# Performance work log

Measured on AMD Instinct MI355X. Metric: run time of the kernel, lower is better.

Reference implementation:

```python
import jax, jax.numpy as jnp
import numpy as np

B, S, H = 32, 512, 768
NH, HD = 8, 96
NC = 3
SEP = 102
NEG = -1e9


def telu(x):
    return x * jnp.tanh(jnp.exp(x))


def setup_inputs() -> dict:
    rng = np.random.default_rng(0)
    key = jax.random.key(0)
    ks = jax.random.split(key, 16)
    # ragged premise/hypothesis spans: [CLS] premise [SEP] hypothesis [SEP] pad
    s1 = rng.integers(64, 256, size=B)
    s2 = rng.integers(s1 + 32, 500)
    ids = rng.integers(1000, 30000, size=(B, S))  # avoid accidental SEP ids
    for i in range(B):
        ids[i, 0] = 101
        ids[i, s1[i]] = SEP
        ids[i, s2[i]] = SEP
        ids[i, s2[i] + 1:] = 0
    pos = np.arange(S)[None, :]
    am = (pos <= s2[:, None]).astype(np.int32)

    def lin(k, i, o):
        return jax.random.normal(k, (i, o), jnp.float32) * 0.02

    return dict(
        hidden_states=jax.random.normal(ks[0], (B, S, H), jnp.float32),
        input_ids=jnp.asarray(ids, jnp.int32),
        attention_mask=jnp.asarray(am, jnp.int32),
        fe_w1=lin(ks[1], H, 512), fe_b1=jnp.zeros(512), fe_g=jnp.ones(512), fe_be=jnp.zeros(512),
        fe_w2=lin(ks[2], 512, 128), fe_b2=jnp.zeros(128),
        al_w1=lin(ks[3], 2 * H, 768), al_b1=jnp.zeros(768),
        al_w2=lin(ks[4], 768, 128), al_b2=jnp.zeros(128),
        mha_wq=lin(ks[5], H, H), mha_bq=jnp.zeros(H),
        mha_wk=lin(ks[6], H, H), mha_bk=jnp.zeros(H),
        mha_wv=lin(ks[7], H, H), mha_bv=jnp.zeros(H),
        mha_wo=lin(ks[8], H, H), mha_bo=jnp.zeros(H),
        dp_w=lin(ks[9], H, 128), dp_b=jnp.zeros(128),
        ap_w=lin(ks[10], H, 128), ap_b=jnp.zeros(128),
        cl_w1=lin(ks[11], 512, 64), cl_b1=jnp.zeros(64),
        cl_w2=lin(ks[12], 64, NC), cl_b2=jnp.zeros(NC),
    )


def reference(hidden_states, input_ids, attention_mask,
              fe_w1, fe_b1, fe_g, fe_be, fe_w2, fe_b2,
              al_w1, al_b1, al_w2, al_b2,
              mha_wq, mha_bq, mha_wk, mha_bk, mha_wv, mha_bv, mha_wo, mha_bo,
              dp_w, dp_b, ap_w, ap_b, cl_w1, cl_b1, cl_w2, cl_b2):
    hs = hidden_states
    am = attention_mask.astype(hs.dtype)
    sep = (input_ids == SEP)
    pos = jnp.arange(S)[None, :]
    s1 = jnp.argmax(sep, axis=1)            # first SEP
    s2 = (S - 1) - jnp.argmax(sep[:, ::-1], axis=1)  # second SEP
    prem = ((pos >= 1) & (pos < s1[:, None])).astype(hs.dtype)   # premise span [1, s1)
    hyp = ((pos > s1[:, None]) & (pos < s2[:, None])).astype(hs.dtype)  # hypothesis (s1, s2)

    def mmean(x, m):  # masked mean over seq: x [B,S,H], m [B,S]
        return jnp.einsum('bsh,bs->bh', x, m) / jnp.clip(m.sum(1, keepdims=True), 1e-9, None)

    # pooled + mean + max representations -> feature_extractor
    pooled = hs[:, 0]
    mean_rep = mmean(hs, am)
    max_rep = jnp.max(jnp.where(am[..., None] > 0, hs, NEG), axis=1)
    h = (pooled + mean_rep + max_rep) @ fe_w1 + fe_b1
    h = (h - h.mean(-1, keepdims=True)) / jnp.sqrt(h.var(-1, keepdims=True) + 1e-5) * fe_g + fe_be
    feat = telu(h @ fe_w2 + fe_b2)

    # sentence diff head
    sent_diff = jnp.abs(mmean(hs, prem) - mmean(hs, hyp))
    diff_rep = telu(sent_diff @ dp_w + dp_b)

    # cross attention: hypothesis queries attend to premise keys/values
    q = (hs @ mha_wq + mha_bq).reshape(B, S, NH, HD)
    k = (hs @ mha_wk + mha_bk).reshape(B, S, NH, HD)
    v = (hs @ mha_wv + mha_bv).reshape(B, S, NH, HD)
    scores = jnp.einsum('bqhd,bkhd->bhqk', q, k) / np.sqrt(HD).astype(np.float32)
    scores = jnp.where(prem[:, None, None, :] > 0, scores, NEG)
    attn = jax.nn.softmax(scores, axis=-1)
    ctx = jnp.einsum('bhqk,bkhd->bqhd', attn, v).reshape(B, S, H) @ mha_wo + mha_bo
    attn_rep = telu(mmean(ctx, hyp) @ ap_w + ap_b)

    # word alignment (both directions share one similarity matrix)
    sim = jnp.einsum('bsd,btd->bst', hs, hs)
    w_p2h = jax.nn.softmax(jnp.where(hyp[:, None, :] > 0, sim, NEG), axis=-1)
    al1 = mmean(jnp.einsum('bst,btd->bsd', w_p2h, hs), prem)
    w_h2p = jax.nn.softmax(jnp.where(prem[:, None, :] > 0, sim, NEG), axis=-1)
    al2 = mmean(jnp.einsum('bst,btd->bsd', w_h2p, hs), hyp)
    align_rep = telu((jnp.concatenate([al1, al2], -1) @ al_w1 + al_b1) @ al_w2 + al_b2)

    combined = jnp.concatenate([feat, diff_rep, attn_rep, align_rep], -1)  # [B, 512]
    logits = telu(combined @ cl_w1 + cl_b1) @ cl_w2 + cl_b2
    return logits
```

## Files before the change

kernel.cpp:

```cpp
#include <hip/hip_runtime.h>
#include <hip/hip_bf16.h>
#include <math.h>

#define SS 512
#define HH 768
#define NEGV -1e9f
#define APAD 100

typedef float f32x4 __attribute__((ext_vector_type(4)));
typedef __bf16 bf16x8 __attribute__((ext_vector_type(8)));

__device__ __forceinline__ float telu_f(float x){ return x * tanhf(expf(x)); }

__device__ __forceinline__ short f2bf(float x){
  __hip_bfloat16 h = __float2bfloat16(x);
  return __builtin_bit_cast(short, h);
}
__device__ __forceinline__ float b2f(short s){
  __hip_bfloat16 h = __builtin_bit_cast(__hip_bfloat16, s);
  return __bfloat162float(h);
}

__device__ __forceinline__ void gl_lds16(const void* g, void* l){
  __builtin_amdgcn_global_load_lds((const __attribute__((address_space(1))) void*)g,
                                   (__attribute__((address_space(3))) void*)l, 16, 0, 0);
}

__device__ __forceinline__ float wred_max(float v){
  #pragma unroll
  for (int o=32;o>0;o>>=1) v = fmaxf(v, __shfl_xor(v, o));
  return v;
}
__device__ __forceinline__ float wred_sum(float v){
  #pragma unroll
  for (int o=32;o>0;o>>=1) v += __shfl_xor(v, o);
  return v;
}

__global__ __launch_bounds__(512) void k_scan(const int* __restrict__ ids, const int* __restrict__ am,
                       int* s1a, int* s2a, float* invnam, float* invnp, float* invnh,
                       float* __restrict__ uacc, float* __restrict__ v1g, float* __restrict__ v2g){
  int b = blockIdx.x, tid = threadIdx.x;
  __shared__ int mn, mx, cnt;
  if (tid==0){ mn = 1<<30; mx = -1; cnt = 0; }
  __syncthreads();
  int id = ids[b*SS+tid];
  if (id==102){ atomicMin(&mn, tid); atomicMax(&mx, tid); }
  atomicAdd(&cnt, am[b*SS+tid]);
  #pragma unroll
  for (int i=0;i<4;i++) uacc[(size_t)b*2048 + tid + i*512] = 0.f;
  v1g[b*SS+tid] = 0.f;
  v2g[b*SS+tid] = 0.f;
  __syncthreads();
  if (tid==0){
    int s1 = mn; if (s1 > 255) s1 = 255; if (s1 < 1) s1 = 1;
    int s2 = mx; if (s2 < s1+1) s2 = s1+1; if (s2 > 511) s2 = 511;
    s1a[b]=s1; s2a[b]=s2;
    invnam[b] = 1.f/fmaxf((float)cnt, 1e-9f);
    invnp[b]  = 1.f/fmaxf((float)(s1-1), 1e-9f);
    invnh[b]  = 1.f/fmaxf((float)(s2-s1-1), 1e-9f);
  }
}

__global__ __launch_bounds__(256) void k_g2(const float* __restrict__ hs, const int* __restrict__ amask,
    const int* __restrict__ s1a, const int* __restrict__ s2a,
    short* __restrict__ hsb, short* __restrict__ hsl, float4* __restrict__ repp,
    const float* __restrict__ wq, const float* __restrict__ wk, const float* __restrict__ wv,
    short* __restrict__ Wt){
  __shared__ __align__(16) char smem[16896];
  int id = blockIdx.x, tid = threadIdx.x;
  if (id < 768){
    int b = id&31, hc = (id>>5)%6, sc = id/192;
    int* ams = (int*)smem;
    float4* rb4 = (float4*)(smem + 512);
    int sbase = sc*128;
    if (tid < 128) ams[tid] = amask[b*SS + sbase + tid];
    __syncthreads();
    int s1 = s1a[b], s2 = s2a[b];
    int hlane = tid & 31, srow = tid >> 5;
    int h0 = hc*128 + hlane*4;
    float sm[4]={0,0,0,0}, sp[4]={0,0,0,0}, sh[4]={0,0,0,0};
    float mxv[4]={NEGV,NEGV,NEGV,NEGV};
    for (int si = srow; si < 128; si += 8){
      int s = sbase + si;
      float4 x = *(const float4*)(hs + ((size_t)(b*SS+s))*HH + h0);
      float xv[4] = {x.x,x.y,x.z,x.w};
      bool am = ams[si] > 0;
      bool ip = (s>=1 && s<s1), ih = (s>s1 && s<s2);
      short hi4[4], lo4[4];
      #pragma unroll
      for (int c=0;c<4;c++){
        if (am){ sm[c]+=xv[c]; mxv[c]=fmaxf(mxv[c],xv[c]); }
        if (ip) sp[c]+=xv[c];
        if (ih) sh[c]+=xv[c];
        hi4[c] = f2bf(xv[c]);
        lo4[c] = f2bf(xv[c] - b2f(hi4[c]));
      }
      *(short4*)(hsb + ((size_t)(b*SS+s))*HH + h0) = *(short4*)hi4;
      *(short4*)(hsl + ((size_t)(b*SS+s))*HH + h0) = *(short4*)lo4;
    }
    #pragma unroll
    for (int c=0;c<4;c++) rb4[srow*128 + hlane*4+c] = make_float4(sm[c], mxv[c], sp[c], sh[c]);
    __syncthreads();
    if (tid < 128){
      float4 a = rb4[tid];
      #pragma unroll
      for (int r=1;r<8;r++){
        float4 v = rb4[r*128 + tid];
        a.x += v.x; a.y = fmaxf(a.y, v.y); a.z += v.z; a.w += v.w;
      }
      repp[(((size_t)(b*6+hc))*4 + sc)*128 + tid] = a;
    }
  } else {
    int w = id - 768;
    int k0 = (w%24)*32, n0 = ((w/24)%24)*32, which = w/576;
    const float* W = which==0? wq : (which==1? wk : wv);
    float (*tl)[33] = (float(*)[33])smem;
    int r = tid>>3, c4 = (tid&7)*4;
    float4 v = *(const float4*)(W + (size_t)(k0+r)*HH + n0 + c4);
    tl[r][c4+0]=v.x; tl[r][c4+1]=v.y; tl[r][c4+2]=v.z; tl[r][c4+3]=v.w;
    __syncthreads();
    short4 o;
    o.x = f2bf(tl[c4+0][r]); o.y = f2bf(tl[c4+1][r]);
    o.z = f2bf(tl[c4+2][r]); o.w = f2bf(tl[c4+3][r]);
    *(short4*)(Wt + (size_t)which*HH*HH + (size_t)(n0+r)*HH + k0 + c4) = o;
  }
}

__device__ __forceinline__ void build_vec(const float4* __restrict__ repp, const float* __restrict__ hs,
    const float* __restrict__ invnam, const float* __restrict__ invnp, const float* __restrict__ invnh,
    int b, int tid, bool want_sdiff, float* xs){
  for (int h = tid; h < HH; h += 256){
    int hc = h>>7, hr = h&127;
    float S=0.f, M=NEGV, P=0.f, Hh=0.f;
    #pragma unroll
    for (int sc=0; sc<4; sc++){
      float4 v = repp[(((size_t)(b*6+hc))*4 + sc)*128 + hr];
      S += v.x; M = fmaxf(M, v.y); P += v.z; Hh += v.w;
    }
    if (want_sdiff) xs[h] = fabsf(P*invnp[b] - Hh*invnh[b]);
    else            xs[h] = hs[((size_t)(b*SS))*HH + h] + S*invnam[b] + M;
  }
}

__global__ __launch_bounds__(256) void k_mm(const short* __restrict__ hsb, const short* __restrict__ hsl,
    const short* __restrict__ Wt,
    const float* __restrict__ bq, const float* __restrict__ bk, const float* __restrict__ bv,
    short* __restrict__ qbh, short* __restrict__ kbh, float* __restrict__ vb,
    const int* __restrict__ s1a, const int* __restrict__ s2a, float* __restrict__ sim,
    const float4* __restrict__ repp, const float* __restrict__ hs,
    const float* __restrict__ invnam, const float* __restrict__ invnp, const float* __restrict__ invnh,
    const float* __restrict__ fe_w1, const float* __restrict__ fe_b1, float* __restrict__ featd,
    const float* __restrict__ dpw, const float* __restrict__ dpb, float* __restrict__ comb){
  __shared__ __align__(16) short smem_s[16384];
  int id = blockIdx.x;
  int tid = threadIdx.x, lane = tid&63, wave = tid>>6;
  int wm = wave>>1, wn = wave&1;
  int lm = lane&15, lq = lane>>4;
  if (id < 320){
    const int TI[10]={0,0,0,0,1,1,1,2,2,3};
    const int TJ[10]={0,1,2,3,1,2,3,2,3,3};
    int b8 = id & 7, q = id >> 3;
    int t = q % 10, bhi = q / 10;
    int b = b8 + 8*bhi;
    int s0 = TI[t]*128, t0 = TJ[t]*128;
    int s2 = s2a[b];
    if (t0 >= s2) return;
    bool diag = (s0 == t0);
    short* Ah = smem_s;
    short* Al = Ah + 4096;
    short* Bh = diag ? Ah : (Ah + 8192);
    short* Bl = diag ? Al : (Ah + 12288);
    const size_t base = (size_t)b*SS*HH;
    f32x4 acc[4][4];
    #pragma unroll
    for (int i=0;i<4;i++)
      #pragma unroll
      for (int j=0;j<4;j++) acc[i][j] = (f32x4){0.f,0.f,0.f,0.f};
    for (int k0=0;k0<HH;k0+=32){
      __syncthreads();
      #pragma unroll
      for (int t2=0;t2<2;t2++){
        int c = tid + t2*256;
        int ib = c>>6, l = c&63;
        int row = ib*16 + (l&15);
        int kk  = k0 + (l>>4)*8;
        gl_lds16(hsb + base + (size_t)(s0+row)*HH + kk, Ah + c*8);
        gl_lds16(hsl + base + (size_t)(s0+row)*HH + kk, Al + c*8);
        if (!diag){
          gl_lds16(hsb + base + (size_t)(t0+row)*HH + kk, Bh + c*8);
          gl_lds16(hsl + base + (size_t)(t0+row)*HH + kk, Bl + c*8);
        }
      }
      __syncthreads();
      bf16x8 ah[4], al[4], bh[4], bl[4];
      #pragma unroll
      for (int i=0;i<4;i++){
        ah[i] = *(const bf16x8*)&Ah[((wm*4+i)*64 + lane)*8];
        al[i] = *(const bf16x8*)&Al[((wm*4+i)*64 + lane)*8];
      }
      #pragma unroll
      for (int j=0;j<4;j++){
        bh[j] = *(const bf16x8*)&Bh[((wn*4+j)*64 + lane)*8];
        bl[j] = *(const bf16x8*)&Bl[((wn*4+j)*64 + lane)*8];
      }
      #pragma unroll
      for (int i=0;i<4;i++)
        #pragma unroll
        for (int j=0;j<4;j++){
          acc[i][j] = __builtin_amdgcn_mfma_f32_16x16x32_bf16(ah[i], bh[j], acc[i][j], 0, 0, 0);
          acc[i][j] = __builtin_amdgcn_mfma_f32_16x16x32_bf16(ah[i], bl[j], acc[i][j], 0, 0, 0);
          acc[i][j] = __builtin_amdgcn_mfma_f32_16x16x32_bf16(al[i], bh[j], acc[i][j], 0, 0, 0);
        }
    }
    #pragma unroll
    for (int i=0;i<4;i++){
      #pragma unroll
      for (int j=0;j<4;j++){
        int col = t0 + wn*64 + j*16 + lm;
        #pragma unroll
        for (int r4=0;r4<4;r4++){
          int row = s0 + wm*64 + i*16 + lq*4 + r4;
          sim[((size_t)(b*SS+row))*SS + col] = acc[i][j][r4];
        }
      }
    }
    if (!diag){
      #pragma unroll
      for (int i=0;i<4;i++){
        #pragma unroll
        for (int j=0;j<4;j++){
          int col  = t0 + wn*64 + j*16 + lm;
          int row0 = s0 + wm*64 + i*16 + lq*4;
          float4 v; v.x=acc[i][j][0]; v.y=acc[i][j][1]; v.z=acc[i][j][2]; v.w=acc[i][j][3];
          *(float4*)(sim + ((size_t)(b*SS+col))*SS + row0) = v;
        }
      }
    }
  } else if (id < 1856){
    int which, local;
    int qid = id - 320;
    if (qid < 768){ which=0; local=qid; }
    else if (qid < 1152){ which=1; local=qid-768; }
    else { which=2; local=qid-1152; }
    int r8 = local & 7, n = (local>>3)%6, gq = local/48;
    int rt = gq*8 + r8;
    int n0 = n*128;
    int r0, b;
    if (which==0){ r0 = rt*128; b = r0>>9; }
    else { b = rt>>1; r0 = b*512 + (rt&1)*128; }
    int s1 = s1a[b], s2 = s2a[b];
    int s0 = r0 & (SS-1);
    if (which==0){ if (s0 >= s2 || s0 + 127 <= s1) return; }
    else { if (s0 >= s1) return; }
    const float* bias = which==0? bq : (which==1? bk : bv);
    const short* Wb = Wt + (size_t)which*HH*HH;
    short* As0 = smem_s;
    short* Bs0 = As0 + 4096;
    short* As1 = As0 + 8192;
    short* Bs1 = As0 + 12288;
    f32x4 acc[4][4];
    #pragma unroll
    for (int i=0;i<4;i++)
      #pragma unroll
      for (int j=0;j<4;j++) acc[i][j] = (f32x4){0.f,0.f,0.f,0.f};
    for (int k0=0;k0<HH;k0+=64){
      __syncthreads();
      #pragma unroll
      for (int t2=0;t2<2;t2++){
        int c = tid + t2*256;
        int ib = c>>6, l = c&63;
        int row = ib*16 + (l&15);
        int kk  = (l>>4)*8;
        gl_lds16(hsb + (size_t)(r0+row)*HH + k0 + kk,      As0 + c*8);
        gl_lds16(Wb  + (size_t)(n0+row)*HH + k0 + kk,      Bs0 + c*8);
        gl_lds16(hsb + (size_t)(r0+row)*HH + k0 + 32 + kk, As1 + c*8);
        gl_lds16(Wb  + (size_t)(n0+row)*HH + k0 + 32 + kk, Bs1 + c*8);
      }
      __syncthreads();
      bf16x8 af[4], bfv[4];
      #pragma unroll
      for (int i=0;i<4;i++) af[i]  = *(const bf16x8*)&As0[((wm*4+i)*64 + lane)*8];
      #pragma unroll
      for (int j=0;j<4;j++) bfv[j] = *(const bf16x8*)&Bs0[((wn*4+j)*64 + lane)*8];
      #pragma unroll
      for (int i=0;i<4;i++)
        #pragma unroll
        for (int j=0;j<4;j++)
          acc[i][j] = __builtin_amdgcn_mfma_f32_16x16x32_bf16(af[i], bfv[j], acc[i][j], 0, 0, 0);
      #pragma unroll
      for (int i=0;i<4;i++) af[i]  = *(const bf16x8*)&As1[((wm*4+i)*64 + lane)*8];
      #pragma unroll
      for (int j=0;j<4;j++) bfv[j] = *(const bf16x8*)&Bs1[((wn*4+j)*64 + lane)*8];
      #pragma unroll
      for (int i=0;i<4;i++)
        #pragma unroll
        for (int j=0;j<4;j++)
          acc[i][j] = __builtin_amdgcn_mfma_f32_16x16x32_bf16(af[i], bfv[j], acc[i][j], 0, 0, 0);
    }
    #pragma unroll
    for (int i=0;i<4;i++){
      #pragma unroll
      for (int j=0;j<4;j++){
        int col = n0 + wn*64 + j*16 + lm;
        float bcol = bias[col];
        #pragma unroll
        for (int r4=0;r4<4;r4++){
          int row = r0 + wm*64 + i*16 + lq*4 + r4;
          int s = row & (SS-1);
          float val = acc[i][j][r4] + bcol;
          if (which==0){
            if (s > s1 && s < s2) qbh[(size_t)row*HH + col] = f2bf(val);
          } else if (s >= 1 && s < s1){
            size_t o = ((size_t)(b*256+s))*HH + col;
            if (which==1) kbh[o] = f2bf(val); else vb[o] = val;
          }
        }
      }
    }
  } else {
    int sid = id - 1856;
    float* xs = (float*)smem_s;
    float* psum = xs + HH;
    int jj = tid & 127, half = tid >> 7;
    if (sid < 128){
      int b = sid&31, j0 = (sid>>5)*128;
      build_vec(repp, hs, invnam, invnp, invnh, b, tid, false, xs);
      __syncthreads();
      float a = 0.f;
      #pragma unroll 8
      for (int i = half*384; i < half*384+384; i++)
        a += xs[i]*fe_w1[(size_t)i*512 + j0 + jj];
      psum[half*128 + jj] = a;
      __syncthreads();
      if (tid < 128)
        featd[(size_t)b*512 + j0 + tid] = fe_b1[j0+tid] + psum[tid] + psum[128+tid];
    } else {
      int b = sid - 128;
      build_vec(repp, hs, invnam, invnp, invnh, b, tid, true, xs);
      __syncthreads();
      float a = 0.f;
      #pragma unroll 8
      for (int i = half*384; i < half*384+384; i++)
        a += xs[i]*dpw[(size_t)i*128 + jj];
      psum[half*128 + jj] = a;
      __syncthreads();
      if (tid < 128)
        comb[b*512 + 128 + tid] = telu_f(dpb[tid] + psum[tid] + psum[128+tid]);
    }
  }
}

__global__ __launch_bounds__(256) void k_attn_simsm(const short* __restrict__ qbh, const short* __restrict__ kbh,
    const int* __restrict__ s1a, const int* __restrict__ s2a, float* __restrict__ uacc,
    const float* __restrict__ sim, float* __restrict__ v1g, float* __restrict__ v2g){
  __shared__ __align__(16) char smem[64000];
  int id = blockIdx.x, tid = threadIdx.x;
  int wave = tid>>6, lane = tid&63;
  if (id < 2048){
    int b = id&31, h = (id>>5)&7, zc = id>>8;
    int s1 = s1a[b], s2 = s2a[b];
    int qs = s1 + 1 + zc*64;
    if (qs >= s2) return;
    short* Ks = (short*)smem;
    short* Qs = Ks + 256*APAD;
    int lm = lane&15, lq = lane>>4;
    int jmax = (s1+15)>>4;
    int krows = jmax<<4;
    for (int i = tid; i < krows*12; i += 256){
      int r = i/12, c = i - r*12;
      *(int4*)&Ks[r*APAD + c*8] = *(const int4*)(kbh + ((size_t)(b*256+r))*HH + h*96 + c*8);
    }
    for (int i = tid; i < 64*12; i += 256){
      int r = i/12, c = i - r*12;
      int q = qs + r;
      int4 v = {0,0,0,0};
      if (q < SS) v = *(const int4*)(qbh + ((size_t)(b*SS+q))*HH + h*96 + c*8);
      *(int4*)&Qs[r*APAD + c*8] = v;
    }
    __syncthreads();
    f32x4 acc[16];
    #pragma unroll
    for (int j=0;j<16;j++) acc[j] = (f32x4){0.f,0.f,0.f,0.f};
    #pragma unroll
    for (int ks=0; ks<3; ks++){
      bf16x8 a = *(const bf16x8*)&Qs[(wave*16+lm)*APAD + ks*32 + lq*8];
      #pragma unroll
      for (int j=0;j<16;j++){
        if (j < jmax){
          bf16x8 bfr = *(const bf16x8*)&Ks[(j*16+lm)*APAD + ks*32 + lq*8];
          acc[j] = __builtin_amdgcn_mfma_f32_16x16x32_bf16(a, bfr, acc[j], 0, 0, 0);
        }
      }
    }
    const float scale = 0.1020620726f;
    float uj[16];
    #pragma unroll
    for (int j=0;j<16;j++) uj[j]=0.f;
    int qrow_base = qs + wave*16 + lq*4;
    #pragma unroll
    for (int r=0;r<4;r++){
      float m = -1e30f;
      float sc[16];
      #pragma unroll
      for (int j=0;j<16;j++){
        int c = j*16 + lm;
        float s = (c>=1 && c<s1) ? acc[j][r]*scale : -1e30f;
        sc[j] = s; m = fmaxf(m, s);
      }
      #pragma unroll
      for (int o=1;o<16;o<<=1) m = fmaxf(m, __shfl_xor(m, o));
      float ssum = 0.f;
      #pragma unroll
      for (int j=0;j<16;j++){ float p = expf(sc[j]-m); sc[j]=p; ssum += p; }
      #pragma unroll
      for (int o=1;o<16;o<<=1) ssum += __shfl_xor(ssum, o);
      bool rvalid = (qrow_base + r) < s2;
      float inv = rvalid ? 1.f/ssum : 0.f;
      #pragma unroll
      for (int j=0;j<16;j++) uj[j] += sc[j]*inv;
    }
    #pragma unroll
    for (int j=0;j<16;j++){
      if (j < jmax){
        float v = uj[j];
        v += __shfl_xor(v, 16);
        v += __shfl_xor(v, 32);
        if (lq==0 && v != 0.f)
          atomicAdd(&uacc[((size_t)(b*8+h))*256 + j*16 + lm], v);
      }
    }
  } else {
    int l = id - 2048;
    int b = l&31, cy = l>>5;
    int s1 = s1a[b], s2 = s2a[b];
    int r0 = cy*64;
    float* av = (float*)smem;
    for (int i=tid;i<2*4*SS;i+=256) av[i]=0.f;
    __syncthreads();
    for (int r = r0 + wave; r < r0+64; r += 4){
      int t0,t1,which;
      if (r>=1 && r<s1){ t0=s1+1; t1=s2; which=0; }
      else if (r>s1 && r<s2){ t0=1; t1=s1; which=1; }
      else continue;
      const float* row = sim + ((size_t)(b*SS+r))*SS;
      float vals[7]; float mx=-1e30f;
      #pragma unroll
      for (int j=0;j<7;j++){
        int t = t0 + lane + 64*j;
        vals[j] = (t<t1) ? row[t] : -1e30f;
        mx = fmaxf(mx, vals[j]);
      }
      mx = wred_max(mx);
      float ssum=0.f;
      #pragma unroll
      for (int j=0;j<7;j++){
        int t = t0+lane+64*j;
        vals[j] = (t<t1)? expf(vals[j]-mx) : 0.f;
        ssum += vals[j];
      }
      ssum = wred_sum(ssum);
      float inv = 1.f/ssum;
      #pragma unroll
      for (int j=0;j<7;j++){
        int t = t0+lane+64*j;
        if (t<t1) av[(which*4 + wave)*SS + t] += vals[j]*inv;
      }
    }
    __syncthreads();
    for (int t=tid;t<SS;t+=256){
      float a0 = av[0*SS+t]+av[1*SS+t]+av[2*SS+t]+av[3*SS+t];
      float a1 = av[4*SS+t]+av[5*SS+t]+av[6*SS+t]+av[7*SS+t];
      if (a0 != 0.f) atomicAdd(&v1g[b*SS+t], a0);
      if (a1 != 0.f) atomicAdd(&v2g[b*SS+t], a1);
    }
  }
}

__global__ __launch_bounds__(256) void k_ctx_alvec(const float* __restrict__ uacc, const float* __restrict__ vb,
    const int* __restrict__ s1a, const float* __restrict__ invnh, float* __restrict__ cmg,
    const float* __restrict__ hs, const float* __restrict__ v1g, const float* __restrict__ v2g,
    const float* __restrict__ invnp, float* __restrict__ catg){
  __shared__ __align__(16) char smem[9216];
  int id = blockIdx.x, tid = threadIdx.x;
  if (id < 192){
    int b = id&31, i0 = (id>>5)*128;
    int s1 = s1a[b]; int nk = s1-1;
    float inh = invnh[b];
    float* us = (float*)smem;
    float* ps = us + 2048;
    for (int idx=tid; idx<2048; idx+=256) us[idx] = uacc[(size_t)b*2048 + idx];
    __syncthreads();
    int ii = tid & 127, half = tid >> 7;
    int i = i0 + ii;
    int h = i/96;
    float a = 0.f;
    int lo = 1 + half*128;
    int hi = nk < (lo+127) ? nk : (lo+127);
    for (int sl=lo; sl<=hi; sl++)
      a += us[h*256+sl]*vb[((size_t)(b*256+sl))*HH + i];
    ps[half*128 + ii] = a;
    __syncthreads();
    if (tid < 128)
      cmg[(size_t)b*HH + i0 + tid] = (ps[tid] + ps[128+tid])*inh;
  } else {
    int l = id - 192;
    int b = l&31, d0 = (l>>5)*64;
    float* sv1 = (float*)smem;
    float* sv2 = sv1 + 512;
    float* p1  = sv2 + 512;
    float* p2  = p1 + 256;
    for (int t=tid;t<SS;t+=256){ sv1[t]=v1g[b*SS+t]; sv2[t]=v2g[b*SS+t]; }
    __syncthreads();
    int d = d0 + (tid&63), ch = tid>>6;
    float a1=0.f, a2=0.f;
    for (int t=ch*128; t<ch*128+128; t++){
      float x = hs[((size_t)(b*SS+t))*HH + d];
      a1 += sv1[t]*x; a2 += sv2[t]*x;
    }
    p1[ch*64 + (tid&63)]=a1; p2[ch*64 + (tid&63)]=a2;
    __syncthreads();
    if (tid < 64){
      float s1_ = p1[tid]+p1[64+tid]+p1[128+tid]+p1[192+tid];
      float s2_ = p2[tid]+p2[64+tid]+p2[128+tid]+p2[192+tid];
      catg[(size_t)b*1536 + d0 + tid]       = s1_*invnp[b];
      catg[(size_t)b*1536 + 768 + d0 + tid] = s2_*invnh[b];
    }
  }
}

template<int K>
__device__ __forceinline__ void gemv_ct(const float* __restrict__ x, const float* __restrict__ W,
    const float* __restrict__ bias, float* __restrict__ y, int b, int j0, int tid,
    float* xs, float* psum){
  for (int i=tid;i<K;i+=256) xs[i] = x[(size_t)b*K + i];
  __syncthreads();
  int jj = tid & 127, half = tid >> 7;
  int j = j0 + jj;
  float a = 0.f;
  #pragma unroll 8
  for (int i = half*(K/2); i < (half+1)*(K/2); i++)
    a += xs[i]*W[(size_t)i*HH + j];
  psum[half*128 + jj] = a;
  __syncthreads();
  if (tid < 128)
    y[(size_t)b*HH + j0 + tid] = bias[j0+tid] + psum[tid] + psum[128+tid];
}

__global__ __launch_bounds__(256) void k_gemvB(const float* __restrict__ cmg, const float* __restrict__ wo,
    const float* __restrict__ bo, float* __restrict__ accg,
    const float* __restrict__ catg, const float* __restrict__ al_w1, const float* __restrict__ al_b1,
    float* __restrict__ tmpg){
  __shared__ float xs[1536];
  __shared__ float psum[256];
  int id = blockIdx.x, tid = threadIdx.x;
  if (id < 192){
    gemv_ct<768>(cmg, wo, bo, accg, id&31, (id>>5)*128, tid, xs, psum);
  } else {
    int l = id-192;
    gemv_ct<1536>(catg, al_w1, al_b1, tmpg, l&31, (l>>5)*128, tid, xs, psum);
  }
}

__global__ __launch_bounds__(256) void k_tailsC(const float* __restrict__ accg, const float* __restrict__ apw,
    const float* __restrict__ apb, const float* __restrict__ tmpg, const float* __restrict__ al_w2,
    const float* __restrict__ al_b2, float* __restrict__ comb,
    const float* __restrict__ featd, const float* __restrict__ g, const float* __restrict__ be,
    const float* __restrict__ w2, const float* __restrict__ b2){
  __shared__ __align__(16) float smem[1664];
  int id = blockIdx.x, tid = threadIdx.x;
  if (id < 64){
    float* xs = smem;
    float* psum = smem + HH;
    const float *x, *W, *bias; int b, off;
    if (id < 32){ b = id; x=accg; W=apw; bias=apb; off=256; }
    else { b = id-32; x=tmpg; W=al_w2; bias=al_b2; off=384; }
    for (int i=tid;i<HH;i+=256) xs[i] = x[(size_t)b*HH + i];
    __syncthreads();
    int jj = tid & 127, half = tid >> 7;
    float a = 0.f;
    #pragma unroll 8
    for (int i = half*384; i < half*384+384; i++)
      a += xs[i]*W[(size_t)i*128 + jj];
    psum[half*128 + jj] = a;
    __syncthreads();
    if (tid < 128)
      comb[b*512 + off + tid] = telu_f(bias[tid] + psum[tid] + psum[128+tid]);
  } else {
    int b = id - 64;
    float* hv  = smem;
    float* hn  = hv + 512;
    float* red = hn + 512;
    float* ps  = red + 256;
    hv[tid] = featd[(size_t)b*512 + tid];
    hv[tid+256] = featd[(size_t)b*512 + tid + 256];
    __syncthreads();
    red[tid] = hv[tid] + hv[tid+256];
    __syncthreads();
    for (int st=128; st>0; st>>=1){ if (tid<st) red[tid]+=red[tid+st]; __syncthreads(); }
    float mean = red[0]*(1.f/512.f);
    __syncthreads();
    float d0 = hv[tid]-mean, d1 = hv[tid+256]-mean;
    red[tid] = d0*d0 + d1*d1;
    __syncthreads();
    for (int st=128; st>0; st>>=1){ if (tid<st) red[tid]+=red[tid+st]; __syncthreads(); }
    float inv = 1.f/sqrtf(red[0]*(1.f/512.f) + 1e-5f);
    __syncthreads();
    hn[tid]     = d0*inv*g[tid]     + be[tid];
    hn[tid+256] = d1*inv*g[tid+256] + be[tid+256];
    __syncthreads();
    int jj = tid & 127, half = tid >> 7;
    float a = 0.f;
    #pragma unroll 8
    for (int k = half*256; k < half*256+256; k++)
      a += hn[k]*w2[k*128 + jj];
    ps[half*128 + jj] = a;
    __syncthreads();
    if (tid < 128)
      comb[b*512 + tid] = telu_f(b2[tid] + ps[tid] + ps[128+tid]);
  }
}

__global__ __launch_bounds__(64) void k_cls(const float* __restrict__ comb,
    const float* __restrict__ w1, const float* __restrict__ b1,
    const float* __restrict__ w2, const float* __restrict__ b2, float* __restrict__ out){
  int b=blockIdx.x, tid=threadIdx.x;
  __shared__ float cb[512];
  __shared__ float t1[64];
  for (int i=tid;i<512;i+=64) cb[i]=comb[b*512+i];
  __syncthreads();
  float a = b1[tid];
  for (int k=0;k<512;k++) a += cb[k]*w1[(size_t)k*64+tid];
  t1[tid]=telu_f(a);
  __syncthreads();
  if (tid<3){
    float o = b2[tid];
    for (int k=0;k<64;k++) o += t1[k]*w2[k*3+tid];
    out[b*3+tid]=o;
  }
}

extern "C" void kernel_launch(void* const* d_in, const int* in_sizes, int n_in,
                              void* d_out, int out_size, void* d_ws, size_t ws_size,
                              hipStream_t stream){
  const float* hs   = (const float*)d_in[0];
  const int*   ids  = (const int*)d_in[1];
  const int*   amask= (const int*)d_in[2];
  const float* fe_w1= (const float*)d_in[3];
  const float* fe_b1= (const float*)d_in[4];
  const float* fe_g = (const float*)d_in[5];
  const float* fe_be= (const float*)d_in[6];
  const float* fe_w2= (const float*)d_in[7];
  const float* fe_b2= (const float*)d_in[8];
  const float* al_w1= (const float*)d_in[9];
  const float* al_b1= (const float*)d_in[10];
  const float* al_w2= (const float*)d_in[11];
  const float* al_b2= (const float*)d_in[12];
  const float* wq   = (const float*)d_in[13];
  const float* bq   = (const float*)d_in[14];
  const float* wk   = (const float*)d_in[15];
  const float* bk   = (const float*)d_in[16];
  const float* wv   = (const float*)d_in[17];
  const float* bv   = (const float*)d_in[18];
  const float* wo   = (const float*)d_in[19];
  const float* bo   = (const float*)d_in[20];
  const float* dpw  = (const float*)d_in[21];
  const float* dpb  = (const float*)d_in[22];
  const float* apw  = (const float*)d_in[23];
  const float* apb  = (const float*)d_in[24];
  const float* clw1 = (const float*)d_in[25];
  const float* clb1 = (const float*)d_in[26];
  const float* clw2 = (const float*)d_in[27];
  const float* clb2 = (const float*)d_in[28];
  float* out = (float*)d_out;

  char* base = (char*)d_ws;
  size_t off = 0;
  auto alloc = [&](size_t bytes)->char*{ char* p = base + off; off += (bytes + 255) & ~(size_t)255; return p; };
  short* hsb  = (short*)alloc((size_t)32*SS*HH*2);
  short* hsl  = (short*)alloc((size_t)32*SS*HH*2);
  short* Wt   = (short*)alloc((size_t)3*HH*HH*2);
  short* qbh  = (short*)alloc((size_t)32*SS*HH*2);
  short* kbh  = (short*)alloc((size_t)32*256*HH*2);
  float* vb   = (float*)alloc((size_t)32*256*HH*4);
  float* simb = (float*)alloc((size_t)32*SS*SS*4);
  float* uacc = (float*)alloc((size_t)32*8*256*4);
  float* v1g  = (float*)alloc((size_t)32*SS*4);
  float* v2g  = (float*)alloc((size_t)32*SS*4);
  int*   s1a  = (int*)alloc(32*4);
  int*   s2a  = (int*)alloc(32*4);
  float* invnam=(float*)alloc(32*4);
  float* invnp =(float*)alloc(32*4);
  float* invnh =(float*)alloc(32*4);
  float* comb = (float*)alloc((size_t)32*512*4);
  float4* repp= (float4*)alloc((size_t)32*6*4*128*16);
  float* featd= (float*)alloc((size_t)32*512*4);
  float* catg = (float*)alloc((size_t)32*1536*4);
  float* tmpg = (float*)alloc((size_t)32*HH*4);
  float* cmg  = (float*)alloc((size_t)32*HH*4);
  float* accg = (float*)alloc((size_t)32*HH*4);

  k_scan<<<dim3(32), dim3(512), 0, stream>>>(ids, amask, s1a, s2a, invnam, invnp, invnh, uacc, v1g, v2g);
  k_g2<<<dim3(2496), dim3(256), 0, stream>>>(hs, amask, s1a, s2a, hsb, hsl, repp, wq, wk, wv, Wt);
  k_mm<<<dim3(2016), dim3(256), 0, stream>>>(hsb, hsl, Wt, bq, bk, bv, qbh, kbh, vb, s1a, s2a, simb,
                                             repp, hs, invnam, invnp, invnh, fe_w1, fe_b1, featd, dpw, dpb, comb);
  k_attn_simsm<<<dim3(2304), dim3(256), 0, stream>>>(qbh, kbh, s1a, s2a, uacc, simb, v1g, v2g);
  k_ctx_alvec<<<dim3(576), dim3(256), 0, stream>>>(uacc, vb, s1a, invnh, cmg, hs, v1g, v2g, invnp, catg);
  k_gemvB<<<dim3(384), dim3(256), 0, stream>>>(cmg, wo, bo, accg, catg, al_w1, al_b1, tmpg);
  k_tailsC<<<dim3(96), dim3(256), 0, stream>>>(accg, apw, apb, tmpg, al_w2, al_b2, comb,
                                               featd, fe_g, fe_be, fe_w2, fe_b2);
  k_cls<<<dim3(32), dim3(64), 0, stream>>>(comb, clw1, clb1, clw2, clb2, out);
}
```

Baseline: 478.5 us.

## Fuse SEP scan and accumulator zeroing into k_g2, skip padded rows

Removes the separate k_scan launch. Each k_g2 reduction block now finds the SEP positions and the mask count for its batch row itself, and one block per batch writes the per-batch scalars. The weight-transpose blocks take over zeroing the accumulator buffers through one contiguous pointer, which assumes uacc, v1g and v2g are allocated back to back. Rows past the second SEP are no longer loaded or converted, and bf16 hi/lo rows are written only for positions before s2. That leaves padding rows of hsb/hsl uninitialised, which is only safe if downstream kernels never read them.

```diff
diff --git a/kernel.cpp b/kernel.cpp
--- a/kernel.cpp
+++ b/kernel.cpp
@@ -37,52 +37,50 @@
   return v;
 }
 
-__global__ __launch_bounds__(512) void k_scan(const int* __restrict__ ids, const int* __restrict__ am,
-                       int* s1a, int* s2a, float* invnam, float* invnp, float* invnh,
-                       float* __restrict__ uacc, float* __restrict__ v1g, float* __restrict__ v2g){
-  int b = blockIdx.x, tid = threadIdx.x;
-  __shared__ int mn, mx, cnt;
-  if (tid==0){ mn = 1<<30; mx = -1; cnt = 0; }
-  __syncthreads();
-  int id = ids[b*SS+tid];
-  if (id==102){ atomicMin(&mn, tid); atomicMax(&mx, tid); }
-  atomicAdd(&cnt, am[b*SS+tid]);
-  #pragma unroll
-  for (int i=0;i<4;i++) uacc[(size_t)b*2048 + tid + i*512] = 0.f;
-  v1g[b*SS+tid] = 0.f;
-  v2g[b*SS+tid] = 0.f;
-  __syncthreads();
-  if (tid==0){
-    int s1 = mn; if (s1 > 255) s1 = 255; if (s1 < 1) s1 = 1;
-    int s2 = mx; if (s2 < s1+1) s2 = s1+1; if (s2 > 511) s2 = 511;
-    s1a[b]=s1; s2a[b]=s2;
-    invnam[b] = 1.f/fmaxf((float)cnt, 1e-9f);
-    invnp[b]  = 1.f/fmaxf((float)(s1-1), 1e-9f);
-    invnh[b]  = 1.f/fmaxf((float)(s2-s1-1), 1e-9f);
-  }
-}
-
-__global__ __launch_bounds__(256) void k_g2(const float* __restrict__ hs, const int* __restrict__ amask,
-    const int* __restrict__ s1a, const int* __restrict__ s2a,
+__global__ __launch_bounds__(256) void k_g2(const float* __restrict__ hs, const int* __restrict__ ids,
+    const int* __restrict__ amask,
     short* __restrict__ hsb, short* __restrict__ hsl, float4* __restrict__ repp,
     const float* __restrict__ wq, const float* __restrict__ wk, const float* __restrict__ wv,
-    short* __restrict__ Wt){
+    short* __restrict__ Wt,
+    int* s1a, int* s2a, float* invnam, float* invnp, float* invnh, float* __restrict__ zacc){
   __shared__ __align__(16) char smem[16896];
+  __shared__ int mn, mx, cnt;
   int id = blockIdx.x, tid = threadIdx.x;
   if (id < 768){
     int b = id&31, hc = (id>>5)%6, sc = id/192;
     int* ams = (int*)smem;
     float4* rb4 = (float4*)(smem + 512);
     int sbase = sc*128;
+    if (tid==0){ mn = 1<<30; mx = -1; cnt = 0; }
+    __syncthreads();
+    {
+      int c2 = 0;
+      #pragma unroll
+      for (int t2=0;t2<2;t2++){
+        int s = tid + t2*256;
+        int idv = ids[b*SS+s];
+        if (idv==102){ atomicMin(&mn, s); atomicMax(&mx, s); }
+        c2 += amask[b*SS+s];
+      }
+      atomicAdd(&cnt, c2);
+    }
     if (tid < 128) ams[tid] = amask[b*SS + sbase + tid];
     __syncthreads();
-    int s1 = s1a[b], s2 = s2a[b];
+    int s1 = mn; if (s1 > 255) s1 = 255; if (s1 < 1) s1 = 1;
+    int s2 = mx; if (s2 < s1+1) s2 = s1+1; if (s2 > 511) s2 = 511;
+    if (hc==0 && sc==0 && tid==0){
+      s1a[b]=s1; s2a[b]=s2;
+      invnam[b] = 1.f/fmaxf((float)cnt, 1e-9f);
+      invnp[b]  = 1.f/fmaxf((float)(s1-1), 1e-9f);
+      invnh[b]  = 1.f/fmaxf((float)(s2-s1-1), 1e-9f);
+    }
     int hlane = tid & 31, srow = tid >> 5;
     int h0 = hc*128 + hlane*4;
     float sm[4]={0,0,0,0}, sp[4]={0,0,0,0}, sh[4]={0,0,0,0};
     float mxv[4]={NEGV,NEGV,NEGV,NEGV};
     for (int si = srow; si < 128; si += 8){
       int s = sbase + si;
+      if (s > s2) continue;
       float4 x = *(const float4*)(hs + ((size_t)(b*SS+s))*HH + h0);
       float xv[4] = {x.x,x.y,x.z,x.w};
       bool am = ams[si] > 0;
@@ -96,8 +94,10 @@
         hi4[c] = f2bf(xv[c]);
         lo4[c] = f2bf(xv[c] - b2f(hi4[c]));
       }
-      *(short4*)(hsb + ((size_t)(b*SS+s))*HH + h0) = *(short4*)hi4;
-      *(short4*)(hsl + ((size_t)(b*SS+s))*HH + h0) = *(short4*)lo4;
+      if (s < s2){
+        *(short4*)(hsb + ((size_t)(b*SS+s))*HH + h0) = *(short4*)hi4;
+        *(short4*)(hsl + ((size_t)(b*SS+s))*HH + h0) = *(short4*)lo4;
+      }
     }
     #pragma unroll
     for (int c=0;c<4;c++) rb4[srow*128 + hlane*4+c] = make_float4(sm[c], mxv[c], sp[c], sh[c]);
@@ -113,6 +113,11 @@
     }
   } else {
     int w = id - 768;
+    if (w < 96){
+      int base = w*1024 + tid;
+      #pragma unroll
+      for (int i=0;i<4;i++) zacc[base + i*256] = 0.f;
+    }
     int k0 = (w%24)*32, n0 = ((w/24)%24)*32, which = w/576;
     const float* W = which==0? wq : (which==1? wk : wv);
     float (*tl)[33] = (float(*)[33])smem;
@@ -700,8 +705,8 @@
   float* cmg  = (float*)alloc((size_t)32*HH*4);
   float* accg = (float*)alloc((size_t)32*HH*4);
 
-  k_scan<<<dim3(32), dim3(512), 0, stream>>>(ids, amask, s1a, s2a, invnam, invnp, invnh, uacc, v1g, v2g);
-  k_g2<<<dim3(2496), dim3(256), 0, stream>>>(hs, amask, s1a, s2a, hsb, hsl, repp, wq, wk, wv, Wt);
+  k_g2<<<dim3(2496), dim3(256), 0, stream>>>(hs, ids, amask, hsb, hsl, repp, wq, wk, wv, Wt,
+                                             s1a, s2a, invnam, invnp, invnh, uacc);
   k_mm<<<dim3(2016), dim3(256), 0, stream>>>(hsb, hsl, Wt, bq, bk, bv, qbh, kbh, vb, s1a, s2a, simb,
                                              repp, hs, invnam, invnp, invnh, fe_w1, fe_b1, featd, dpw, dpb, comb);
   k_attn_simsm<<<dim3(2304), dim3(256), 0, stream>>>(qbh, kbh, s1a, s2a, uacc, simb, v1g, v2g);
```

Result: slower. 502.7 us (+5.1%).
